# Kernel tuning notes

Hardware: AMD Instinct MI355X
Metric: run time of the kernel (lower is better)

Reference implementation:

```python
import jax, jax.numpy as jnp
import numpy as np

N_NODES = 50000
N_EDGES = 800000
IN_DIM, HID_DIM, LAT_DIM = 512, 512, 128


def _glorot(key, shape):
    fan_in = shape[0]
    return jax.random.normal(key, shape, dtype=jnp.float32) / np.sqrt(fan_in)


def setup_inputs() -> dict:
    key = jax.random.key(0)
    ks = jax.random.split(key, 10)
    x = jax.random.normal(ks[0], (N_NODES, IN_DIM), dtype=jnp.float32)
    edge_index = jax.random.randint(ks[1], (2, N_EDGES), 0, N_NODES, dtype=jnp.int64)
    edge_weight = jax.random.uniform(ks[2], (N_EDGES,), dtype=jnp.float32)
    return {
        "x": x,
        "edge_index": edge_index,
        "edge_weight": edge_weight,
        "W1": _glorot(ks[3], (IN_DIM, HID_DIM)), "b1": jnp.zeros((HID_DIM,), jnp.float32),
        "W2": _glorot(ks[4], (HID_DIM, LAT_DIM)), "b2": jnp.zeros((LAT_DIM,), jnp.float32),
        "W3": _glorot(ks[5], (LAT_DIM, HID_DIM)), "b3": jnp.zeros((HID_DIM,), jnp.float32),
        "W4": _glorot(ks[6], (HID_DIM, IN_DIM)), "b4": jnp.zeros((IN_DIM,), jnp.float32),
    }


def gcn_conv(x, W, b, src, dst, ew, n_nodes):
    """PyG GCNConv: out = D^{-1/2}(A+I)D^{-1/2} X W + b, self-loop weight 1."""
    xw = x @ W  # [N, out_dim]
    # degree over edges + self-loops (self-loop weight = 1)
    deg = jax.ops.segment_sum(ew, dst, num_segments=n_nodes) + 1.0  # [N]
    dinv = jnp.where(deg > 0, jax.lax.rsqrt(deg), 0.0)
    norm = dinv[src] * ew * dinv[dst]  # [E]
    msg = norm[:, None] * xw[src]      # [E, out_dim] per-edge gather
    agg = jax.ops.segment_sum(msg, dst, num_segments=n_nodes)  # scatter-add
    agg = agg + (dinv * dinv)[:, None] * xw  # self-loop contribution
    return agg + b


def reference(x, edge_index, edge_weight, W1, b1, W2, b2, W3, b3, W4, b4):
    src, dst = edge_index[0], edge_index[1]
    n = x.shape[0]
    # encode
    h = jax.nn.relu(gcn_conv(x, W1, b1, src, dst, edge_weight, n))
    z = gcn_conv(h, W2, b2, src, dst, edge_weight, n)
    # decode (dropout is identity in eval mode)
    h2 = jax.nn.relu(gcn_conv(z, W3, b3, src, dst, edge_weight, n))
    x_recon = gcn_conv(h2, W4, b4, src, dst, edge_weight, n)
    return (x_recon, z)
```

## Files before the change

### kernel.cpp

```cpp
#include <hip/hip_runtime.h>


typedef short bf16x8 __attribute__((ext_vector_type(8)));
typedef float f32x4 __attribute__((ext_vector_type(4)));

__device__ __forceinline__ float bf2f(unsigned short u) {
  return __uint_as_float(((unsigned int)u) << 16);
}
__device__ __forceinline__ unsigned short f2bf(float f) {
  unsigned int u = __float_as_uint(f);
  return (unsigned short)((u + 0x7fffu + ((u >> 16) & 1u)) >> 16);
}

__device__ __forceinline__ void gload_lds16(const void* g, void* l) {
  __builtin_amdgcn_global_load_lds(
      (const __attribute__((address_space(1))) unsigned int*)g,
      (__attribute__((address_space(3))) unsigned int*)l, 16, 0, 0);
}


__global__ void deg_hist_kernel(const int* __restrict__ dst, const float* __restrict__ ew,
                                float* __restrict__ deg, int* __restrict__ cnt, int E) {
  int e = blockIdx.x * blockDim.x + threadIdx.x;
  if (e >= E) return;
  int d = dst[e];
  atomicAdd(&deg[d], ew[e]);
  atomicAdd(&cnt[d], 1);
}

__global__ void dinv_kernel(const float* __restrict__ deg, float* __restrict__ dinv, int n) {
  int i = blockIdx.x * blockDim.x + threadIdx.x;
  if (i >= n) return;
  dinv[i] = rsqrtf(deg[i] + 1.0f);
}

__global__ void block_sums_kernel(const int* __restrict__ cnt, int* __restrict__ sums, int n) {
  __shared__ int sh[512];
  int i = blockIdx.x * 512 + threadIdx.x;
  sh[threadIdx.x] = (i < n) ? cnt[i] : 0;
  __syncthreads();
  for (int s = 256; s > 0; s >>= 1) {
    if (threadIdx.x < s) sh[threadIdx.x] += sh[threadIdx.x + s];
    __syncthreads();
  }
  if (threadIdx.x == 0) sums[blockIdx.x] = sh[0];
}

__global__ void scan_sums_kernel(int* sums, int nb) {
  if (threadIdx.x == 0 && blockIdx.x == 0) {
    int acc = 0;
    for (int i = 0; i < nb; ++i) { int v = sums[i]; sums[i] = acc; acc += v; }
  }
}

__global__ void scan_final_kernel(const int* __restrict__ cnt, const int* __restrict__ sums,
                                  int* __restrict__ rowPtr, int* __restrict__ fill, int n) {
  __shared__ int sh[512];
  int i = blockIdx.x * 512 + threadIdx.x;
  int v = (i < n) ? cnt[i] : 0;
  sh[threadIdx.x] = v;
  __syncthreads();
  for (int off = 1; off < 512; off <<= 1) {
    int y = (threadIdx.x >= off) ? sh[threadIdx.x - off] : 0;
    __syncthreads();
    sh[threadIdx.x] += y;
    __syncthreads();
  }
  if (i < n) {
    int incl = sh[threadIdx.x];
    int base = sums[blockIdx.x];
    int excl = base + incl - v;
    rowPtr[i] = excl;
    fill[i] = excl;
    if (i == n - 1) rowPtr[n] = base + incl;
  }
}

__global__ void scatter_edges_kernel(const int* __restrict__ src, const int* __restrict__ dst,
                                     const float* __restrict__ ew, const float* __restrict__ dinv,
                                     int* __restrict__ fill, int2* __restrict__ pk, int E) {
  int e = blockIdx.x * blockDim.x + threadIdx.x;
  if (e >= E) return;
  int s = src[e], d = dst[e];
  int p = atomicAdd(&fill[d], 1);
  float v = dinv[s] * ew[e] * dinv[d];
  pk[p] = make_int2(s, __float_as_int(v));
}


__global__ void cvt_x_kernel(const float* __restrict__ x, unsigned short* __restrict__ xbf,
                             int n, int Mpad) {
  int g = blockIdx.x * 256 + threadIdx.x;
  int total = Mpad * 64;
  if (g >= total) return;
  int row = g >> 6;
  int cc = (g & 63) << 3;
  bf16x8 o;
  if (row < n) {
    const float* p = x + (size_t)row * 512 + cc;
    float4 f0 = *(const float4*)p;
    float4 f1 = *(const float4*)(p + 4);
    o[0] = (short)f2bf(f0.x); o[1] = (short)f2bf(f0.y);
    o[2] = (short)f2bf(f0.z); o[3] = (short)f2bf(f0.w);
    o[4] = (short)f2bf(f1.x); o[5] = (short)f2bf(f1.y);
    o[6] = (short)f2bf(f1.z); o[7] = (short)f2bf(f1.w);
  } else {
#pragma unroll
    for (int j = 0; j < 8; ++j) o[j] = 0;
  }
  *(bf16x8*)(xbf + (size_t)g * 8) = o;
}


__global__ void tile_w_kernel(const float* __restrict__ W, short* __restrict__ hi,
                              int K, int N) {
  int g = blockIdx.x * 256 + threadIdx.x;
  int kb_cnt = K >> 6;
  int total = (N >> 7) * kb_cnt * 1024;
  if (g >= total) return;
  int c = g & 1023;
  int t = g >> 10;
  int kb = t % kb_cnt;
  int nb = t / kb_cnt;
  int colg = (nb << 7) + (c >> 3);
  int k0 = (kb << 6) + (((c & 7) ^ ((c >> 3) & 7)) << 3);
  bf16x8 h8;
#pragma unroll
  for (int j = 0; j < 8; ++j) {
    float w = W[(size_t)(k0 + j) * N + colg];
    h8[j] = (short)f2bf(w);
  }
  *(bf16x8*)(hi + (size_t)g * 8) = h8;
}


template <int BN, bool BIAS, bool RELU>
__global__ __launch_bounds__(2 * BN) void mfma_gemm(
    const unsigned short* __restrict__ A, const short* __restrict__ Bhi,
    const float* __restrict__ bias, unsigned short* __restrict__ C, int N, int K) {
  constexpr int W = BN / 32;
  constexpr int RW = 128 / W;
  constexpr int IA = RW / 8;
  constexpr int NH = BN / 128;
  constexpr int WH = W / NH;
  constexpr int CW = BN / 64;

  __shared__ short As[8192];
  __shared__ short Bs[BN * 64];

  const int tid = threadIdx.x;
  const int lane = tid & 63;
  const int wave = tid >> 6;
  const int rowblk = blockIdx.y << 7;
  const int colblk = blockIdx.x * BN;
  const int wr = (wave / CW) << 6;
  const int wc = (wave % CW) << 6;
  const int lr = lane & 15;
  const int lk = lane >> 4;
  const int kbN = K >> 6;
  const int half = wave / WH;
  const int wh = wave % WH;
  const int nb0 = colblk >> 7;

  f32x4 acc[4][4];
#pragma unroll
  for (int i = 0; i < 4; ++i)
#pragma unroll
    for (int j = 0; j < 4; ++j) {
      f32x4 z = {0.f, 0.f, 0.f, 0.f};
      acc[i][j] = z;
    }

  const int arow = wave * RW + (lane >> 3);
  const size_t abase = (size_t)(rowblk + arow) * K + (size_t)(((lane & 7) ^ ((lane >> 3) & 7)) << 3);
  short* AsW = As + wave * (RW * 64);
  short* BsW = Bs + half * 8192 + wh * 2048;

  for (int kb = 0; kb < kbN; ++kb) {
    const unsigned short* asrc = A + abase + (kb << 6);
    const short* bsrc = Bhi + ((size_t)(nb0 + half) * kbN + kb) * 8192 + (size_t)(wh * 256 + lane) * 8;
#pragma unroll
    for (int i = 0; i < IA; ++i)
      gload_lds16(asrc + (size_t)(i * 8) * K, AsW + i * 512);
#pragma unroll
    for (int i = 0; i < 4; ++i)
      gload_lds16(bsrc + i * 512, BsW + i * 512);
    __syncthreads();
#pragma unroll
    for (int kk = 0; kk < 2; ++kk) {
      bf16x8 af[4], bhf[4];
      const int kc = kk * 4 + lk;
#pragma unroll
      for (int rb = 0; rb < 4; ++rb) {
        int rowl = wr + rb * 16 + lr;
        af[rb] = *(const bf16x8*)(As + rowl * 64 + ((kc ^ (rowl & 7)) << 3));
      }
#pragma unroll
      for (int cb = 0; cb < 4; ++cb) {
        int coll = wc + cb * 16 + lr;
        bhf[cb] = *(const bf16x8*)(Bs + coll * 64 + ((kc ^ (coll & 7)) << 3));
      }
#pragma unroll
      for (int rb = 0; rb < 4; ++rb)
#pragma unroll
        for (int cb = 0; cb < 4; ++cb)
          acc[rb][cb] = __builtin_amdgcn_mfma_f32_16x16x32_bf16(af[rb], bhf[cb], acc[rb][cb], 0, 0, 0);
    }
    __syncthreads();
  }

#pragma unroll
  for (int cb = 0; cb < 4; ++cb) {
    int colg = colblk + wc + cb * 16 + lr;
    float badd = BIAS ? bias[colg] : 0.0f;
#pragma unroll
    for (int rb = 0; rb < 4; ++rb) {
#pragma unroll
      for (int i = 0; i < 4; ++i) {
        int row = rowblk + wr + rb * 16 + lk * 4 + i;
        float v = acc[rb][cb][i] + badd;
        if (RELU) v = fmaxf(v, 0.f);
        C[(size_t)row * N + colg] = f2bf(v);
      }
    }
  }
}


template <int PT, bool INF32>
__device__ __forceinline__ void load_row(const void* p, size_t off, float* xv) {
  if (INF32) {
    if (PT == 2) {
      float2 f = *(const float2*)((const float*)p + off);
      xv[0] = f.x; xv[1] = f.y;
    } else {
      float4 f0 = *(const float4*)((const float*)p + off);
      float4 f1 = *(const float4*)((const float*)p + off + 4);
      xv[0] = f0.x; xv[1] = f0.y; xv[2] = f0.z; xv[3] = f0.w;
      xv[4] = f1.x; xv[5] = f1.y; xv[6] = f1.z; xv[7] = f1.w;
    }
  } else {
    if (PT == 2) {
      unsigned int u = *(const unsigned int*)((const unsigned short*)p + off);
      xv[0] = bf2f((unsigned short)(u & 0xffffu));
      xv[1] = bf2f((unsigned short)(u >> 16));
    } else {
      bf16x8 r = *(const bf16x8*)((const short*)p + off);
#pragma unroll
      for (int j = 0; j < 8; ++j) xv[j] = bf2f((unsigned short)r[j]);
    }
  }
}

template <int PT, bool INF32, bool BIAS, bool RELU, bool W32, bool W16>
__global__ __launch_bounds__(256) void agg_kernel(
    const void* __restrict__ xw, const int2* __restrict__ pk,
    const int* __restrict__ rowPtr, const float* __restrict__ dinv,
    const float* __restrict__ bias, float* __restrict__ out32,
    unsigned short* __restrict__ out16, int n) {
  const int DIM = PT * 64;
  int node = blockIdx.x * 4 + (threadIdx.x >> 6);
  if (node >= n) return;
  int t = threadIdx.x & 63;
  float acc[PT];
#pragma unroll
  for (int q = 0; q < PT; ++q) acc[q] = 0.f;

  int beg = rowPtr[node], end = rowPtr[node + 1];
  int e = beg;
  for (; e + 4 <= end; e += 4) {
    int2 p0 = pk[e + 0], p1 = pk[e + 1], p2 = pk[e + 2], p3 = pk[e + 3];
    float x0[PT], x1[PT], x2[PT], x3[PT];
    load_row<PT, INF32>(xw, (size_t)p0.x * DIM + t * PT, x0);
    load_row<PT, INF32>(xw, (size_t)p1.x * DIM + t * PT, x1);
    load_row<PT, INF32>(xw, (size_t)p2.x * DIM + t * PT, x2);
    load_row<PT, INF32>(xw, (size_t)p3.x * DIM + t * PT, x3);
    float v0 = __int_as_float(p0.y), v1 = __int_as_float(p1.y);
    float v2 = __int_as_float(p2.y), v3 = __int_as_float(p3.y);
#pragma unroll
    for (int q = 0; q < PT; ++q)
      acc[q] += v0 * x0[q] + v1 * x1[q] + v2 * x2[q] + v3 * x3[q];
  }
  for (; e < end; ++e) {
    int2 pe = pk[e];
    float v = __int_as_float(pe.y);
    float xv[PT];
    load_row<PT, INF32>(xw, (size_t)pe.x * DIM + t * PT, xv);
#pragma unroll
    for (int q = 0; q < PT; ++q) acc[q] += v * xv[q];
  }
  float di = dinv[node];
  float sl = di * di;
  {
    float xv[PT];
    load_row<PT, INF32>(xw, (size_t)node * DIM + t * PT, xv);
#pragma unroll
    for (int q = 0; q < PT; ++q) acc[q] += sl * xv[q];
  }
  if (BIAS) {
#pragma unroll
    for (int q = 0; q < PT; ++q) acc[q] += bias[t * PT + q];
  }
  if (RELU) {
#pragma unroll
    for (int q = 0; q < PT; ++q) acc[q] = fmaxf(acc[q], 0.f);
  }
  if (W32) {
    if (PT == 2) {
      float2 o; o.x = acc[0]; o.y = acc[1];
      *(float2*)(out32 + (size_t)node * DIM + t * PT) = o;
    } else {
      float4 o0, o1;
      o0.x = acc[0]; o0.y = acc[1]; o0.z = acc[2]; o0.w = acc[3];
      o1.x = acc[4 % PT]; o1.y = acc[5 % PT]; o1.z = acc[6 % PT]; o1.w = acc[7 % PT];
      *(float4*)(out32 + (size_t)node * DIM + t * PT) = o0;
      *(float4*)(out32 + (size_t)node * DIM + t * PT + 4) = o1;
    }
  }
  if (W16) {
    if (PT == 2) {
      unsigned int u = (unsigned int)f2bf(acc[0]) | ((unsigned int)f2bf(acc[1]) << 16);
      *(unsigned int*)(out16 + (size_t)node * DIM + t * PT) = u;
    } else {
      bf16x8 o;
#pragma unroll
      for (int j = 0; j < PT; ++j) o[j % 8] = (short)f2bf(acc[j]);
      *(bf16x8*)(out16 + (size_t)node * DIM + t * PT) = o;
    }
  }
}


extern "C" void kernel_launch(void* const* d_in, const int* in_sizes, int n_in,
                              void* d_out, int out_size, void* d_ws, size_t ws_size,
                              hipStream_t stream) {
  const float* x  = (const float*)d_in[0];
  const int*   ei = (const int*)d_in[1];
  const float* ew = (const float*)d_in[2];
  const float* W1 = (const float*)d_in[3];
  const float* b1 = (const float*)d_in[4];
  const float* W2 = (const float*)d_in[5];
  const float* b2 = (const float*)d_in[6];
  const float* W3 = (const float*)d_in[7];
  const float* b3 = (const float*)d_in[8];
  const float* W4 = (const float*)d_in[9];
  const float* b4 = (const float*)d_in[10];

  const int n = in_sizes[0] / 512;
  const int E = in_sizes[2];
  const int MB128 = (n + 127) / 128;
  const int Mpad = MB128 * 128;

  float* out   = (float*)d_out;
  float* z_out = out + (size_t)n * 512;

  char* w = (char*)d_ws;
  auto alloc = [&](size_t bytes) {
    char* p = w;
    w += (bytes + 255) & ~(size_t)255;
    return p;
  };
  float* deg    = (float*)alloc((size_t)n * 4);
  float* dinv   = (float*)alloc((size_t)n * 4);
  int*   cnt    = (int*)alloc((size_t)n * 4);
  int*   rowPtr = (int*)alloc((size_t)(n + 1) * 4);
  int*   fill   = (int*)alloc((size_t)n * 4);
  int*   sums   = (int*)alloc(4096);
  int2*  pk     = (int2*)alloc((size_t)E * 8);
  short* whi1 = (short*)alloc((size_t)512 * 512 * 2);
  short* whi2 = (short*)alloc((size_t)512 * 128 * 2);
  short* whi3 = (short*)alloc((size_t)128 * 512 * 2);
  short* whi4 = (short*)alloc((size_t)512 * 512 * 2);
  unsigned short* T  = (unsigned short*)alloc((size_t)Mpad * 128 * 2);
  unsigned short* B1 = (unsigned short*)alloc((size_t)Mpad * 512 * 2);
  unsigned short* B2 = (unsigned short*)alloc((size_t)Mpad * 512 * 2);

  unsigned short* zbf = B2;

  const int* srcp = ei;
  const int* dstp = ei + E;

  hipMemsetAsync(deg, 0, (size_t)n * 4, stream);
  hipMemsetAsync(cnt, 0, (size_t)n * 4, stream);
  deg_hist_kernel<<<(E + 255) / 256, 256, 0, stream>>>(dstp, ew, deg, cnt, E);
  dinv_kernel<<<(n + 255) / 256, 256, 0, stream>>>(deg, dinv, n);
  int NB = (n + 511) / 512;
  block_sums_kernel<<<NB, 512, 0, stream>>>(cnt, sums, n);
  scan_sums_kernel<<<1, 64, 0, stream>>>(sums, NB);
  scan_final_kernel<<<NB, 512, 0, stream>>>(cnt, sums, rowPtr, fill, n);
  scatter_edges_kernel<<<(E + 255) / 256, 256, 0, stream>>>(srcp, dstp, ew, dinv, fill, pk, E);

  tile_w_kernel<<<(4 * 8 * 1024 + 255) / 256, 256, 0, stream>>>(W1, whi1, 512, 512);
  tile_w_kernel<<<(1 * 8 * 1024 + 255) / 256, 256, 0, stream>>>(W2, whi2, 512, 128);
  tile_w_kernel<<<(4 * 2 * 1024 + 255) / 256, 256, 0, stream>>>(W3, whi3, 128, 512);
  tile_w_kernel<<<(4 * 8 * 1024 + 255) / 256, 256, 0, stream>>>(W4, whi4, 512, 512);
  cvt_x_kernel<<<(Mpad * 64 + 255) / 256, 256, 0, stream>>>(x, B1, n, Mpad);

  const int AGB = (n + 3) / 4;

  mfma_gemm<256, false, false><<<dim3(2, MB128), 512, 0, stream>>>(B1, whi1, nullptr, B2, 512, 512);
  agg_kernel<8, false, true, true, false, true><<<AGB, 256, 0, stream>>>(
      B2, pk, rowPtr, dinv, b1, nullptr, B1, n);

  mfma_gemm<128, false, false><<<dim3(1, MB128), 256, 0, stream>>>(B1, whi2, nullptr, T, 128, 512);
  agg_kernel<2, false, true, false, true, true><<<AGB, 256, 0, stream>>>(
      T, pk, rowPtr, dinv, b2, z_out, zbf, n);

  agg_kernel<2, false, false, false, false, true><<<AGB, 256, 0, stream>>>(
      zbf, pk, rowPtr, dinv, nullptr, nullptr, T, n);
  mfma_gemm<256, true, true><<<dim3(2, MB128), 512, 0, stream>>>(T, whi3, b3, B2, 512, 128);

  mfma_gemm<256, false, false><<<dim3(2, MB128), 512, 0, stream>>>(B2, whi4, nullptr, B1, 512, 512);
  agg_kernel<8, false, true, false, true, false><<<AGB, 256, 0, stream>>>(
      B1, pk, rowPtr, dinv, b4, out, nullptr, n);
}
```

Baseline: 640.8 us.

## Fuse x fp32-to-bf16 conversion into first GEMM, parallelize scan, tune agg unroll

Removes the separate cvt_x kernel by having the first GEMM load fp32 rows of x, convert them to bf16 in registers and store them into LDS, with row indices clamped for padding. This drops a full write and reread of the bf16 copy of x. The single-threaded block-sum scan becomes a 512-thread shared-memory scan. The aggregation kernel gets a templated unroll factor, set to 8 for the 128-wide layers to expose more independent gathers. The risk is that the fused A path loses asynchronous global-to-LDS loads and adds conversion work inside the GEMM loop.

```diff
diff --git a/kernel.cpp b/kernel.cpp
--- a/kernel.cpp
+++ b/kernel.cpp
@@ -47,10 +47,18 @@
 }
 
 __global__ void scan_sums_kernel(int* sums, int nb) {
-  if (threadIdx.x == 0 && blockIdx.x == 0) {
-    int acc = 0;
-    for (int i = 0; i < nb; ++i) { int v = sums[i]; sums[i] = acc; acc += v; }
-  }
+  __shared__ int sh[512];
+  int t = threadIdx.x;
+  int v = (t < nb) ? sums[t] : 0;
+  sh[t] = v;
+  __syncthreads();
+  for (int off = 1; off < 512; off <<= 1) {
+    int y = (t >= off) ? sh[t - off] : 0;
+    __syncthreads();
+    sh[t] += y;
+    __syncthreads();
+  }
+  if (t < nb) sums[t] = sh[t] - v;
 }
 
 __global__ void scan_final_kernel(const int* __restrict__ cnt, const int* __restrict__ sums,
@@ -85,30 +93,6 @@
   int p = atomicAdd(&fill[d], 1);
   float v = dinv[s] * ew[e] * dinv[d];
   pk[p] = make_int2(s, __float_as_int(v));
-}
-
-
-__global__ void cvt_x_kernel(const float* __restrict__ x, unsigned short* __restrict__ xbf,
-                             int n, int Mpad) {
-  int g = blockIdx.x * 256 + threadIdx.x;
-  int total = Mpad * 64;
-  if (g >= total) return;
-  int row = g >> 6;
-  int cc = (g & 63) << 3;
-  bf16x8 o;
-  if (row < n) {
-    const float* p = x + (size_t)row * 512 + cc;
-    float4 f0 = *(const float4*)p;
-    float4 f1 = *(const float4*)(p + 4);
-    o[0] = (short)f2bf(f0.x); o[1] = (short)f2bf(f0.y);
-    o[2] = (short)f2bf(f0.z); o[3] = (short)f2bf(f0.w);
-    o[4] = (short)f2bf(f1.x); o[5] = (short)f2bf(f1.y);
-    o[6] = (short)f2bf(f1.z); o[7] = (short)f2bf(f1.w);
-  } else {
-#pragma unroll
-    for (int j = 0; j < 8; ++j) o[j] = 0;
-  }
-  *(bf16x8*)(xbf + (size_t)g * 8) = o;
 }
 
 
@@ -134,10 +118,11 @@
 }
 
 
-template <int BN, bool BIAS, bool RELU>
+template <int BN, bool AF32, bool BIAS, bool RELU>
 __global__ __launch_bounds__(2 * BN) void mfma_gemm(
-    const unsigned short* __restrict__ A, const short* __restrict__ Bhi,
-    const float* __restrict__ bias, unsigned short* __restrict__ C, int N, int K) {
+    const void* __restrict__ Aptr, const short* __restrict__ Bhi,
+    const float* __restrict__ bias, unsigned short* __restrict__ C,
+    int M, int N, int K) {
   constexpr int W = BN / 32;
   constexpr int RW = 128 / W;
   constexpr int IA = RW / 8;
@@ -171,20 +156,37 @@
       acc[i][j] = z;
     }
 
-  const int arow = wave * RW + (lane >> 3);
-  const size_t abase = (size_t)(rowblk + arow) * K + (size_t)(((lane & 7) ^ ((lane >> 3) & 7)) << 3);
+  size_t aoff[IA];
+#pragma unroll
+  for (int i = 0; i < IA; ++i) {
+    int rg = rowblk + wave * RW + i * 8 + (lane >> 3);
+    if (AF32) rg = (rg < M) ? rg : (M - 1);
+    aoff[i] = (size_t)rg * K + (size_t)(((lane & 7) ^ ((lane >> 3) & 7)) << 3);
+  }
   short* AsW = As + wave * (RW * 64);
   short* BsW = Bs + half * 8192 + wh * 2048;
 
   for (int kb = 0; kb < kbN; ++kb) {
-    const unsigned short* asrc = A + abase + (kb << 6);
     const short* bsrc = Bhi + ((size_t)(nb0 + half) * kbN + kb) * 8192 + (size_t)(wh * 256 + lane) * 8;
-#pragma unroll
-    for (int i = 0; i < IA; ++i)
-      gload_lds16(asrc + (size_t)(i * 8) * K, AsW + i * 512);
 #pragma unroll
     for (int i = 0; i < 4; ++i)
       gload_lds16(bsrc + i * 512, BsW + i * 512);
+#pragma unroll
+    for (int i = 0; i < IA; ++i) {
+      if (AF32) {
+        const float* ap = (const float*)Aptr + aoff[i] + (kb << 6);
+        float4 f0 = *(const float4*)ap;
+        float4 f1 = *(const float4*)(ap + 4);
+        bf16x8 t;
+        t[0] = (short)f2bf(f0.x); t[1] = (short)f2bf(f0.y);
+        t[2] = (short)f2bf(f0.z); t[3] = (short)f2bf(f0.w);
+        t[4] = (short)f2bf(f1.x); t[5] = (short)f2bf(f1.y);
+        t[6] = (short)f2bf(f1.z); t[7] = (short)f2bf(f1.w);
+        *(bf16x8*)(AsW + i * 512 + lane * 8) = t;
+      } else {
+        gload_lds16((const unsigned short*)Aptr + aoff[i] + (kb << 6), AsW + i * 512);
+      }
+    }
     __syncthreads();
 #pragma unroll
     for (int kk = 0; kk < 2; ++kk) {
@@ -252,7 +254,7 @@
   }
 }
 
-template <int PT, bool INF32, bool BIAS, bool RELU, bool W32, bool W16>
+template <int PT, int UF, bool INF32, bool BIAS, bool RELU, bool W32, bool W16>
 __global__ __launch_bounds__(256) void agg_kernel(
     const void* __restrict__ xw, const int2* __restrict__ pk,
     const int* __restrict__ rowPtr, const float* __restrict__ dinv,
@@ -268,18 +270,20 @@
 
   int beg = rowPtr[node], end = rowPtr[node + 1];
   int e = beg;
-  for (; e + 4 <= end; e += 4) {
-    int2 p0 = pk[e + 0], p1 = pk[e + 1], p2 = pk[e + 2], p3 = pk[e + 3];
-    float x0[PT], x1[PT], x2[PT], x3[PT];
-    load_row<PT, INF32>(xw, (size_t)p0.x * DIM + t * PT, x0);
-    load_row<PT, INF32>(xw, (size_t)p1.x * DIM + t * PT, x1);
-    load_row<PT, INF32>(xw, (size_t)p2.x * DIM + t * PT, x2);
-    load_row<PT, INF32>(xw, (size_t)p3.x * DIM + t * PT, x3);
-    float v0 = __int_as_float(p0.y), v1 = __int_as_float(p1.y);
-    float v2 = __int_as_float(p2.y), v3 = __int_as_float(p3.y);
-#pragma unroll
-    for (int q = 0; q < PT; ++q)
-      acc[q] += v0 * x0[q] + v1 * x1[q] + v2 * x2[q] + v3 * x3[q];
+  for (; e + UF <= end; e += UF) {
+    int2 p[UF];
+    float xv[UF][PT];
+#pragma unroll
+    for (int u = 0; u < UF; ++u) p[u] = pk[e + u];
+#pragma unroll
+    for (int u = 0; u < UF; ++u)
+      load_row<PT, INF32>(xw, (size_t)p[u].x * DIM + t * PT, xv[u]);
+#pragma unroll
+    for (int u = 0; u < UF; ++u) {
+      float v = __int_as_float(p[u].y);
+#pragma unroll
+      for (int q = 0; q < PT; ++q) acc[q] += v * xv[u][q];
+    }
   }
   for (; e < end; ++e) {
     int2 pe = pk[e];
@@ -386,7 +390,7 @@
   dinv_kernel<<<(n + 255) / 256, 256, 0, stream>>>(deg, dinv, n);
   int NB = (n + 511) / 512;
   block_sums_kernel<<<NB, 512, 0, stream>>>(cnt, sums, n);
-  scan_sums_kernel<<<1, 64, 0, stream>>>(sums, NB);
+  scan_sums_kernel<<<1, 512, 0, stream>>>(sums, NB);
   scan_final_kernel<<<NB, 512, 0, stream>>>(cnt, sums, rowPtr, fill, n);
   scatter_edges_kernel<<<(E + 255) / 256, 256, 0, stream>>>(srcp, dstp, ew, dinv, fill, pk, E);
 
@@ -394,23 +398,26 @@
   tile_w_kernel<<<(1 * 8 * 1024 + 255) / 256, 256, 0, stream>>>(W2, whi2, 512, 128);
   tile_w_kernel<<<(4 * 2 * 1024 + 255) / 256, 256, 0, stream>>>(W3, whi3, 128, 512);
   tile_w_kernel<<<(4 * 8 * 1024 + 255) / 256, 256, 0, stream>>>(W4, whi4, 512, 512);
-  cvt_x_kernel<<<(Mpad * 64 + 255) / 256, 256, 0, stream>>>(x, B1, n, Mpad);
 
   const int AGB = (n + 3) / 4;
 
-  mfma_gemm<256, false, false><<<dim3(2, MB128), 512, 0, stream>>>(B1, whi1, nullptr, B2, 512, 512);
-  agg_kernel<8, false, true, true, false, true><<<AGB, 256, 0, stream>>>(
+  mfma_gemm<256, true, false, false><<<dim3(2, MB128), 512, 0, stream>>>(
+      x, whi1, nullptr, B2, n, 512, 512);
+  agg_kernel<8, 4, false, true, true, false, true><<<AGB, 256, 0, stream>>>(
       B2, pk, rowPtr, dinv, b1, nullptr, B1, n);
 
-  mfma_gemm<128, false, false><<<dim3(1, MB128), 256, 0, stream>>>(B1, whi2, nullptr, T, 128, 512);
-  agg_kernel<2, false, true, false, true, true><<<AGB, 256, 0, stream>>>(
+  mfma_gemm<128, false, false, false><<<dim3(1, MB128), 256, 0, stream>>>(
+      B1, whi2, nullptr, T, Mpad, 128, 512);
+  agg_kernel<2, 8, false, true, false, true, true><<<AGB, 256, 0, stream>>>(
       T, pk, rowPtr, dinv, b2, z_out, zbf, n);
 
-  agg_kernel<2, false, false, false, false, true><<<AGB, 256, 0, stream>>>(
+  agg_kernel<2, 8, false, false, false, false, true><<<AGB, 256, 0, stream>>>(
       zbf, pk, rowPtr, dinv, nullptr, nullptr, T, n);
-  mfma_gemm<256, true, true><<<dim3(2, MB128), 512, 0, stream>>>(T, whi3, b3, B2, 512, 128);
-
-  mfma_gemm<256, false, false><<<dim3(2, MB128), 512, 0, stream>>>(B2, whi4, nullptr, B1, 512, 512);
-  agg_kernel<8, false, true, false, true, false><<<AGB, 256, 0, stream>>>(
+  mfma_gemm<256, false, true, true><<<dim3(2, MB128), 512, 0, stream>>>(
+      T, whi3, b3, B2, Mpad, 512, 128);
+
+  mfma_gemm<256, false, false, false><<<dim3(2, MB128), 512, 0, stream>>>(
+      B2, whi4, nullptr, B1, Mpad, 512, 512);
+  agg_kernel<8, 4, false, true, false, true, false><<<AGB, 256, 0, stream>>>(
       B1, pk, rowPtr, dinv, b4, out, nullptr, n);
 }
```

Result: faster. 617.2 us (-3.7%).
